# Performance work log

Hardware: AMD Instinct MI355X
Metric: run time of the kernel (lower is better)

## Reference

```python
import jax, jax.numpy as jnp
import numpy as np

SCALE = 0.08838834764831845  # 1/sqrt(head_dim=128)


def setup_inputs() -> dict:
    key = jax.random.key(0)
    ks = jax.random.split(key, 6)
    B, H, KH, D, S = 16, 32, 8, 128, 8192
    q = jax.random.normal(ks[0], (B, H, D), dtype=jnp.float32)
    k = jax.random.normal(ks[1], (B, KH, D), dtype=jnp.float32)
    v = jax.random.normal(ks[2], (B, KH, D), dtype=jnp.float32)
    k_cache = jax.random.normal(ks[3], (B, S, KH, D), dtype=jnp.float32)
    v_cache = jax.random.normal(ks[4], (B, S, KH, D), dtype=jnp.float32)
    slot_mapping = jax.random.randint(ks[5], (B,), 0, S, dtype=jnp.int64)
    return {"q": q, "k": k, "v": v, "k_cache": k_cache,
            "v_cache": v_cache, "slot_mapping": slot_mapping}


def reference(q, k, v, k_cache, v_cache, slot_mapping):
    # Decode-stage paged attention with GQA.
    # q: [B, H, D]; k,v: [B, KH, D]; caches: [B, S, KH, D]; slot_mapping: [B]
    B, H, D = q.shape
    KH = k.shape[1]
    G = H // KH  # num_queries_per_kv
    b_idx = jnp.arange(B)
    # store_kvcache: scatter new k/v into cache at per-sequence slots
    kc = k_cache.at[b_idx, slot_mapping].set(k)
    vc = v_cache.at[b_idx, slot_mapping].set(v)
    # GQA attention without repeat_interleave: group query heads per kv head
    qg = q.reshape(B, KH, G, D)
    scores = jnp.einsum('bkgd,bskd->bkgs', qg, kc) * SCALE  # [B,KH,G,S]
    w = jax.nn.softmax(scores, axis=-1)
    out = jnp.einsum('bkgs,bskd->bkgd', w, vc)              # [B,KH,G,D]
    return out.reshape(B, H * D)
```

## Files before the change

### kernel.cpp

```cpp
#include <hip/hip_runtime.h>

#define NB 16
#define NH 32
#define NKH 8
#define NG 4
#define ND 128
#define NS 8192
#define ROWF 1024
#define SC2 (0.08838834764831845f * 1.44269504088896340736f)

typedef float f4v __attribute__((ext_vector_type(4)));

__device__ __forceinline__ int load_slot(const int* __restrict__ sm, int b) {
    bool is64 = true;
#pragma unroll
    for (int i = 0; i < 8; ++i) is64 = is64 && (sm[2 * i + 1] == 0);
    return is64 ? sm[2 * b] : sm[b];
}

__device__ __forceinline__ void loadp(
    int s, int slot, const float* __restrict__ kbase,
    const float* __restrict__ vbase, const float* __restrict__ krow_new,
    const float* __restrict__ vrow_new, f4v& ka, f4v& kb, f4v& vv)
{
    const float* kp = (s == slot) ? krow_new : (kbase + (size_t)s * ROWF);
    const float* vp = (s == slot) ? vrow_new : (vbase + (size_t)s * ROWF);
    ka = ((const f4v*)kp)[0];
    kb = ((const f4v*)kp)[1];
    vv = __builtin_nontemporal_load((const f4v*)vp);
}

__device__ __forceinline__ void step(
    const f4v& ka, const f4v& kb, const f4v& vv,
    const f4v* __restrict__ qa, const f4v* __restrict__ qb,
    float* __restrict__ l, f4v* __restrict__ acc)
{
    float t[NG];
#pragma unroll
    for (int g = 0; g < NG; ++g)
        t[g] = ka.x * qa[g].x + ka.y * qa[g].y + ka.z * qa[g].z + ka.w * qa[g].w
             + kb.x * qb[g].x + kb.y * qb[g].y + kb.z * qb[g].z + kb.w * qb[g].w;
#pragma unroll
    for (int g = 0; g < NG; ++g) t[g] += __shfl_xor(t[g], 8);
#pragma unroll
    for (int g = 0; g < NG; ++g) t[g] += __shfl_xor(t[g], 4);
#pragma unroll
    for (int g = 0; g < NG; ++g) t[g] += __shfl_xor(t[g], 2);
#pragma unroll
    for (int g = 0; g < NG; ++g) t[g] += __shfl_xor(t[g], 1);
#pragma unroll
    for (int g = 0; g < NG; ++g) {
        const float p = exp2f(t[g] * SC2);
        l[g] += p;
        acc[g] += vv * p;
    }
}

__global__ __launch_bounds__(1024, 4) void attn_fused(
    const float* __restrict__ qin, const float* __restrict__ knew,
    const float* __restrict__ vnew, const float* __restrict__ kc,
    const float* __restrict__ vc, const int* __restrict__ slot_map,
    float* __restrict__ out)
{
    const int bid   = blockIdx.x;
    const int pair  = bid & 127;
    const int dhalf = bid >> 7;
    const int kh = pair & 7;
    const int b  = pair >> 3;
    const int tid  = threadIdx.x;
    const int wave = tid >> 6;
    const int lane = tid & 63;
    const int quarter = lane >> 4;
    const int il   = lane & 15;
    const int dk0  = il * 8;
    const int dv0  = dhalf * 64 + il * 4;

    const int slot = load_slot(slot_map, b);

    f4v qa[NG], qb[NG];
#pragma unroll
    for (int g = 0; g < NG; ++g) {
        const float* qrow = qin + ((size_t)(b * NH + kh * NG + g)) * ND + dk0;
        qa[g] = *(const f4v*)(qrow);
        qb[g] = *(const f4v*)(qrow + 4);
    }

    const float* kbase = kc + (size_t)b * NS * ROWF + (size_t)kh * ND + dk0;
    const float* vbase = vc + (size_t)b * NS * ROWF + (size_t)kh * ND + dv0;
    const float* krow_new = knew + ((size_t)(b * NKH + kh)) * ND + dk0;
    const float* vrow_new = vnew + ((size_t)(b * NKH + kh)) * ND + dv0;

    float l[NG];
    f4v acc[NG];
#pragma unroll
    for (int g = 0; g < NG; ++g) {
        l[g] = 0.f;
        acc[g] = (f4v)(0.f);
    }

    const int s0 = wave * 4 + quarter;

    f4v kaA, kbA, vvA, kaB, kbB, vvB, kaC, kbC, vvC;
    loadp(s0,      slot, kbase, vbase, krow_new, vrow_new, kaA, kbA, vvA);
    loadp(s0 + 64, slot, kbase, vbase, krow_new, vrow_new, kaB, kbB, vvB);

#pragma unroll 1
    for (int i = 0; i <= 123; i += 3) {
        loadp(s0 + (i + 2) * 64, slot, kbase, vbase, krow_new, vrow_new, kaC, kbC, vvC);
        step(kaA, kbA, vvA, qa, qb, l, acc);
        loadp(s0 + (i + 3) * 64, slot, kbase, vbase, krow_new, vrow_new, kaA, kbA, vvA);
        step(kaB, kbB, vvB, qa, qb, l, acc);
        loadp(s0 + (i + 4) * 64, slot, kbase, vbase, krow_new, vrow_new, kaB, kbB, vvB);
        step(kaC, kbC, vvC, qa, qb, l, acc);
    }
    step(kaA, kbA, vvA, qa, qb, l, acc);
    step(kaB, kbB, vvB, qa, qb, l, acc);

#pragma unroll
    for (int g = 0; g < NG; ++g) {
        l[g] += __shfl_xor(l[g], 16);
        l[g] += __shfl_xor(l[g], 32);
#pragma unroll
        for (int c = 0; c < 4; ++c) {
            float x = acc[g][c];
            x += __shfl_xor(x, 16);
            x += __shfl_xor(x, 32);
            acc[g][c] = x;
        }
    }

    __shared__ float s_acc[16][NG][64];
    __shared__ float s_l[16][NG];
    if (quarter == 0) {
#pragma unroll
        for (int g = 0; g < NG; ++g)
            *(f4v*)&s_acc[wave][g][il * 4] = acc[g];
        if (il == 0) {
#pragma unroll
            for (int g = 0; g < NG; ++g) s_l[wave][g] = l[g];
        }
    }
    __syncthreads();

    if (tid < NG * 64) {
        const int g  = tid >> 6;
        const int dd = tid & 63;
        float L = 0.f, o = 0.f;
#pragma unroll
        for (int w = 0; w < 16; ++w) {
            L += s_l[w][g];
            o += s_acc[w][g][dd];
        }
        out[((size_t)(b * NH + kh * NG + g)) * ND + dhalf * 64 + dd] = o / L;
    }
}

extern "C" void kernel_launch(void* const* d_in, const int* in_sizes, int n_in,
                              void* d_out, int out_size, void* d_ws, size_t ws_size,
                              hipStream_t stream) {
    const float* q  = (const float*)d_in[0];
    const float* k  = (const float*)d_in[1];
    const float* v  = (const float*)d_in[2];
    const float* kc = (const float*)d_in[3];
    const float* vc = (const float*)d_in[4];
    const int* slot = (const int*)d_in[5];
    float* out = (float*)d_out;
    (void)d_ws; (void)ws_size; (void)in_sizes; (void)n_in; (void)out_size;

    attn_fused<<<dim3(256), dim3(1024), 0, stream>>>(q, k, v, kc, vc, slot, out);
}
```

Measured before the change: 186.2 us.

## Split sequence across two blocks with workspace merge instead of splitting head dim

Replaces the head-dim split, where each block read the full K row but only half of V, with a split-K over the sequence. Each of two blocks handles half of the sequence over the full head dimension and writes partial sums and denominators to workspace. A second small kernel then merges the halves. This removes the duplicate K reads, since the old layout loaded every K row twice across the two d-halves, at the cost of an extra launch and a workspace round-trip.

Result: faster. 172.6 us (-7.3%).

```diff
diff --git a/kernel.cpp b/kernel.cpp
--- a/kernel.cpp
+++ b/kernel.cpp
@@ -16,6 +16,151 @@
 #pragma unroll
     for (int i = 0; i < 8; ++i) is64 = is64 && (sm[2 * i + 1] == 0);
     return is64 ? sm[2 * b] : sm[b];
+}
+
+__device__ __forceinline__ void loadp2(
+    int s, int slot, const float* __restrict__ kbase,
+    const float* __restrict__ vbase, const float* __restrict__ krow_new,
+    const float* __restrict__ vrow_new, f4v& kv, f4v& vv)
+{
+    const float* kp = (s == slot) ? krow_new : (kbase + (size_t)s * ROWF);
+    const float* vp = (s == slot) ? vrow_new : (vbase + (size_t)s * ROWF);
+    kv = __builtin_nontemporal_load((const f4v*)kp);
+    vv = __builtin_nontemporal_load((const f4v*)vp);
+}
+
+__device__ __forceinline__ void step2(
+    const f4v& kv, const f4v& vv, const f4v* __restrict__ q,
+    float* __restrict__ l, f4v* __restrict__ acc)
+{
+    float t[NG];
+#pragma unroll
+    for (int g = 0; g < NG; ++g)
+        t[g] = kv.x * q[g].x + kv.y * q[g].y + kv.z * q[g].z + kv.w * q[g].w;
+#pragma unroll
+    for (int g = 0; g < NG; ++g) t[g] += __shfl_xor(t[g], 16);
+#pragma unroll
+    for (int g = 0; g < NG; ++g) t[g] += __shfl_xor(t[g], 8);
+#pragma unroll
+    for (int g = 0; g < NG; ++g) t[g] += __shfl_xor(t[g], 4);
+#pragma unroll
+    for (int g = 0; g < NG; ++g) t[g] += __shfl_xor(t[g], 2);
+#pragma unroll
+    for (int g = 0; g < NG; ++g) t[g] += __shfl_xor(t[g], 1);
+#pragma unroll
+    for (int g = 0; g < NG; ++g) {
+        const float p = exp2f(t[g] * SC2);
+        l[g] += p;
+        acc[g] += vv * p;
+    }
+}
+
+__global__ __launch_bounds__(1024, 4) void attn_partial(
+    const float* __restrict__ qin, const float* __restrict__ knew,
+    const float* __restrict__ vnew, const float* __restrict__ kc,
+    const float* __restrict__ vc, const int* __restrict__ slot_map,
+    float* __restrict__ wsacc,
+    float* __restrict__ wsl)
+{
+    const int bid   = blockIdx.x;
+    const int shalf = bid & 1;
+    const int pair  = bid >> 1;
+    const int kh = pair & 7;
+    const int b  = pair >> 3;
+    const int tid  = threadIdx.x;
+    const int wave = tid >> 6;
+    const int lane = tid & 63;
+    const int half = lane >> 5;
+    const int il   = lane & 31;
+    const int d0   = il * 4;
+
+    const int slot = load_slot(slot_map, b);
+
+    f4v q[NG];
+#pragma unroll
+    for (int g = 0; g < NG; ++g)
+        q[g] = *(const f4v*)(qin + ((size_t)(b * NH + kh * NG + g)) * ND + d0);
+
+    const float* kbase = kc + (size_t)b * NS * ROWF + (size_t)kh * ND + d0;
+    const float* vbase = vc + (size_t)b * NS * ROWF + (size_t)kh * ND + d0;
+    const float* krow_new = knew + ((size_t)(b * NKH + kh)) * ND + d0;
+    const float* vrow_new = vnew + ((size_t)(b * NKH + kh)) * ND + d0;
+
+    float l[NG];
+    f4v acc[NG];
+#pragma unroll
+    for (int g = 0; g < NG; ++g) { l[g] = 0.f; acc[g] = (f4v)(0.f); }
+
+    const int s0 = shalf * (NS / 2) + wave * 2 + half;
+
+    f4v kA, vA, kB, vB, kC, vC;
+    loadp2(s0,      slot, kbase, vbase, krow_new, vrow_new, kA, vA);
+    loadp2(s0 + 32, slot, kbase, vbase, krow_new, vrow_new, kB, vB);
+
+#pragma unroll 1
+    for (int i = 0; i <= 123; i += 3) {
+        loadp2(s0 + (i + 2) * 32, slot, kbase, vbase, krow_new, vrow_new, kC, vC);
+        step2(kA, vA, q, l, acc);
+        loadp2(s0 + (i + 3) * 32, slot, kbase, vbase, krow_new, vrow_new, kA, vA);
+        step2(kB, vB, q, l, acc);
+        loadp2(s0 + (i + 4) * 32, slot, kbase, vbase, krow_new, vrow_new, kB, vB);
+        step2(kC, vC, q, l, acc);
+    }
+    step2(kA, vA, q, l, acc);
+    step2(kB, vB, q, l, acc);
+
+#pragma unroll
+    for (int g = 0; g < NG; ++g) {
+        l[g] += __shfl_xor(l[g], 32);
+#pragma unroll
+        for (int c = 0; c < 4; ++c) {
+            float x = acc[g][c];
+            x += __shfl_xor(x, 32);
+            acc[g][c] = x;
+        }
+    }
+
+    __shared__ float s_acc[16][NG][ND];
+    __shared__ float s_l[16][NG];
+    if (half == 0) {
+#pragma unroll
+        for (int g = 0; g < NG; ++g)
+            *(f4v*)&s_acc[wave][g][d0] = acc[g];
+        if (il == 0) {
+#pragma unroll
+            for (int g = 0; g < NG; ++g) s_l[wave][g] = l[g];
+        }
+    }
+    __syncthreads();
+
+    if (tid < NG * ND) {
+        const int g  = tid >> 7;
+        const int dd = tid & 127;
+        float L = 0.f, o = 0.f;
+#pragma unroll
+        for (int w = 0; w < 16; ++w) {
+            L += s_l[w][g];
+            o += s_acc[w][g][dd];
+        }
+        wsacc[((size_t)bid * NG + g) * ND + dd] = o;
+        if (dd == 0) wsl[bid * NG + g] = L;
+    }
+}
+
+__global__ __launch_bounds__(512) void attn_merge(
+    const float* __restrict__ wsacc, const float* __restrict__ wsl,
+    float* __restrict__ out)
+{
+    const int pair = blockIdx.x;
+    const int kh = pair & 7;
+    const int b  = pair >> 3;
+    const int tid = threadIdx.x;
+    const int g  = tid >> 7;
+    const int dd = tid & 127;
+    const float o = wsacc[((size_t)(pair * 2) * NG + g) * ND + dd]
+                  + wsacc[((size_t)(pair * 2 + 1) * NG + g) * ND + dd];
+    const float L = wsl[(pair * 2) * NG + g] + wsl[(pair * 2 + 1) * NG + g];
+    out[((size_t)(b * NH + kh * NG + g)) * ND + dd] = o / L;
 }
 
 __device__ __forceinline__ void loadp(
@@ -93,10 +238,7 @@
     float l[NG];
     f4v acc[NG];
 #pragma unroll
-    for (int g = 0; g < NG; ++g) {
-        l[g] = 0.f;
-        acc[g] = (f4v)(0.f);
-    }
+    for (int g = 0; g < NG; ++g) { l[g] = 0.f; acc[g] = (f4v)(0.f); }
 
     const int s0 = wave * 4 + quarter;
 
@@ -165,7 +307,16 @@
     const float* vc = (const float*)d_in[4];
     const int* slot = (const int*)d_in[5];
     float* out = (float*)d_out;
-    (void)d_ws; (void)ws_size; (void)in_sizes; (void)n_in; (void)out_size;
-
-    attn_fused<<<dim3(256), dim3(1024), 0, stream>>>(q, k, v, kc, vc, slot, out);
-}
+    (void)in_sizes; (void)n_in; (void)out_size;
+
+    const size_t need = ((size_t)256 * NG * ND + 256 * NG) * sizeof(float);
+    if (ws_size >= need) {
+        float* wsacc = (float*)d_ws;
+        float* wsl   = wsacc + (size_t)256 * NG * ND;
+        attn_partial<<<dim3(256), dim3(1024), 0, stream>>>(
+            q, k, v, kc, vc, slot, wsacc, wsl);
+        attn_merge<<<dim3(128), dim3(512), 0, stream>>>(wsacc, wsl, out);
+    } else {
+        attn_fused<<<dim3(256), dim3(1024), 0, stream>>>(q, k, v, kc, vc, slot, out);
+    }
+}
```
